# Kernel optimization log

Hardware: AMD Instinct MI355X
Metric: run time of the kernel (lower is better)

The kernel has to match this reference:

```python
import jax, jax.numpy as jnp
import numpy as np

H = 16          # num_heads
OUT = 256       # out_channels; projection width = 5*OUT
LN_EPS = 1e-5


def setup_inputs() -> dict:
    key = jax.random.key(0)
    ks = jax.random.split(key, 8)
    B, T, C = 2, 2048, 1024
    P = 5 * OUT
    sc = 1.0 / np.sqrt(C)
    x = jax.random.normal(ks[0], (B, T, C), dtype=jnp.float32)
    Wq = jax.random.normal(ks[1], (C, C), dtype=jnp.float32) * sc
    Wk = jax.random.normal(ks[2], (C, C), dtype=jnp.float32) * sc
    Wv = jax.random.normal(ks[3], (C, C), dtype=jnp.float32) * sc
    bq = jnp.zeros((C,), jnp.float32)
    bk = jnp.zeros((C,), jnp.float32)
    bv = jnp.zeros((C,), jnp.float32)
    gamma = jnp.zeros((1,), jnp.float32)  # nn.Parameter(torch.zeros(1))
    Wp = jax.random.normal(ks[4], (C, P), dtype=jnp.float32) * sc
    bp = jnp.zeros((P,), jnp.float32)
    ln_g = jnp.ones((P,), jnp.float32)
    ln_b = jnp.zeros((P,), jnp.float32)
    bez_p = jnp.array([0.0, 0.0, 1.0, 1.0], jnp.float32)  # cubic Bezier control points
    return dict(x=x, Wq=Wq, bq=bq, Wk=Wk, bk=bk, Wv=Wv, bv=bv, gamma=gamma,
                Wp=Wp, bp=bp, ln_g=ln_g, ln_b=ln_b, bez_p=bez_p)


def _bezier(z, p):
    # cubic Bezier evaluated at s = sigmoid(z), scalar control points p[0..3]
    s = jax.nn.sigmoid(z)
    u = 1.0 - s
    return (u * u * u) * p[0] + 3.0 * (u * u) * s * p[1] + 3.0 * u * (s * s) * p[2] + (s * s * s) * p[3]


def reference(x, Wq, bq, Wk, bk, Wv, bv, gamma, Wp, bp, ln_g, ln_b, bez_p):
    B, T, C = x.shape
    D = C // H
    # QKV projections -> [B, H, T, D]
    q = (x @ Wq + bq).reshape(B, T, H, D).transpose(0, 2, 1, 3)
    k = (x @ Wk + bk).reshape(B, T, H, D).transpose(0, 2, 1, 3)
    v = (x @ Wv + bv).reshape(B, T, H, D).transpose(0, 2, 1, 3)
    # scaled dot-product attention, full [B,H,T,T] scores (as in source)
    attn = jax.nn.softmax(jnp.einsum('bhtd,bhsd->bhts', q, k) / (D ** 0.5), axis=-1)
    out = jnp.einsum('bhts,bhsd->bhtd', attn, v).transpose(0, 2, 1, 3).reshape(B, T, C)
    out = gamma * out + x  # gated residual
    # projection: Linear -> LayerNorm -> BezierActivation
    h = out @ Wp + bp
    mu = jnp.mean(h, axis=-1, keepdims=True)
    var = jnp.mean(jnp.square(h - mu), axis=-1, keepdims=True)
    h = (h - mu) * jax.lax.rsqrt(var + LN_EPS) * ln_g + ln_b
    return _bezier(h, bez_p)
```

## Files before the change

### kernel.cpp

```cpp
#include <hip/hip_runtime.h>
#include <hip/hip_bf16.h>
#include <math.h>


#define H_ 16
#define D_ 64
#define B_ 2
#define T_ 2048
#define C_ 1024
#define P_ 1280
#define M_ 4096

#define PREP_CAST0 1280
#define PREP_QKV0  2304
#define PREP_GRID  5376

typedef __bf16 bf16_t;
typedef __bf16 v8bf __attribute__((ext_vector_type(8)));
typedef __bf16 v4bf __attribute__((ext_vector_type(4)));
typedef float  v4f  __attribute__((ext_vector_type(4)));

__device__ __forceinline__ void gload_lds16(const void* g, void* l) {
  __builtin_amdgcn_global_load_lds((const __attribute__((address_space(1))) void*)g,
                                   (__attribute__((address_space(3))) void*)l, 16, 0, 0);
}

__device__ __forceinline__ void stage64x64(const bf16_t* __restrict__ g, bf16_t* lds, int tid) {
#pragma unroll
  for (int i = 0; i < 2; ++i) {
    int off  = i * 4096 + tid * 16;
    int row  = off >> 7;
    int colb = off & 127;
    const char* gp = (const char*)g + (size_t)row * 2048 + colb;
    char* lp = (char*)lds + i * 4096 + (tid >> 6) * 1024;
    gload_lds16(gp, lp);
  }
}

template<int LD>
__device__ __forceinline__ void stage_tile128x32(const bf16_t* __restrict__ g, bf16_t* lds, int tid) {
#pragma unroll
  for (int i = 0; i < 2; ++i) {
    int off  = i * 4096 + tid * 16;
    int row  = off >> 6;
    int colb = off & 63;
    const char* gp = (const char*)(g + row * LD) + colb;
    char* lp = (char*)lds + i * 4096 + (tid >> 6) * 1024;
    gload_lds16(gp, lp);
  }
}

__device__ __forceinline__ void stage_f32_tile(const float* __restrict__ src, bf16_t* lds, int tid) {
  int row = tid >> 1, half = tid & 1;
  const float* xp = src + (size_t)row * C_ + half * 16;
  float4 f0 = *(const float4*)(xp);
  float4 f1 = *(const float4*)(xp + 4);
  float4 f2 = *(const float4*)(xp + 8);
  float4 f3 = *(const float4*)(xp + 12);
  v8bf lo = {(__bf16)f0.x, (__bf16)f0.y, (__bf16)f0.z, (__bf16)f0.w,
             (__bf16)f1.x, (__bf16)f1.y, (__bf16)f1.z, (__bf16)f1.w};
  v8bf hi = {(__bf16)f2.x, (__bf16)f2.y, (__bf16)f2.z, (__bf16)f2.w,
             (__bf16)f3.x, (__bf16)f3.y, (__bf16)f3.z, (__bf16)f3.w};
  *(v8bf*)(lds + row * 32 + half * 16)     = lo;
  *(v8bf*)(lds + row * 32 + half * 16 + 8) = hi;
}

__global__ __launch_bounds__(256) void prep_kernel(const float* __restrict__ Wp, bf16_t* __restrict__ WpT,
                                                   const float* __restrict__ x, bf16_t* __restrict__ pa,
                                                   const float* __restrict__ Wq, const float* __restrict__ Wk,
                                                   const float* __restrict__ Wv, bf16_t* __restrict__ WT,
                                                   const float* __restrict__ gamma) {
  __shared__ float tile[32][33];
  const int bid = blockIdx.x;
  const float* src;
  bf16_t* dst;
  int N, tile_id;
  if (bid < PREP_CAST0) {
    src = Wp; dst = WpT; N = P_; tile_id = bid;
  } else if (bid < PREP_QKV0) {
    int base = ((bid - PREP_CAST0) * 256 + threadIdx.x) * 16;
    float4 f0 = *(const float4*)(x + base);
    float4 f1 = *(const float4*)(x + base + 4);
    float4 f2 = *(const float4*)(x + base + 8);
    float4 f3 = *(const float4*)(x + base + 12);
    v8bf lo = {(__bf16)f0.x, (__bf16)f0.y, (__bf16)f0.z, (__bf16)f0.w,
               (__bf16)f1.x, (__bf16)f1.y, (__bf16)f1.z, (__bf16)f1.w};
    v8bf hi = {(__bf16)f2.x, (__bf16)f2.y, (__bf16)f2.z, (__bf16)f2.w,
               (__bf16)f3.x, (__bf16)f3.y, (__bf16)f3.z, (__bf16)f3.w};
    *(v8bf*)(pa + base)     = lo;
    *(v8bf*)(pa + base + 8) = hi;
    return;
  } else {
    if (gamma[0] == 0.0f) return;
    int b2 = bid - PREP_QKV0;
    int w = b2 >> 10;
    tile_id = b2 & 1023;
    src = (w == 0) ? Wq : (w == 1) ? Wk : Wv;
    dst = WT + (size_t)w * C_ * C_;
    N = C_;
  }
  const int nt = N / 32;
  const int n0 = (tile_id % nt) * 32, k0 = (tile_id / nt) * 32;
  const int tx = threadIdx.x & 31, ty = threadIdx.x >> 5;
#pragma unroll
  for (int i = 0; i < 32; i += 8)
    tile[ty + i][tx] = src[(size_t)(k0 + ty + i) * N + n0 + tx];
  __syncthreads();
#pragma unroll
  for (int i = 0; i < 32; i += 8)
    dst[(size_t)(n0 + ty + i) * C_ + k0 + tx] = (bf16_t)tile[tx][ty + i];
}

__global__ __launch_bounds__(256) void gemm_qkv(const float* __restrict__ x,
                                                const bf16_t* __restrict__ WT,
                                                const float* __restrict__ bq,
                                                const float* __restrict__ bk,
                                                const float* __restrict__ bv,
                                                bf16_t* __restrict__ q, bf16_t* __restrict__ k,
                                                bf16_t* __restrict__ v,
                                                const float* __restrict__ gamma) {
  if (gamma[0] == 0.0f) return;
  __shared__ alignas(16) bf16_t sA[128 * 32];
  __shared__ alignas(16) bf16_t sB[128 * 32];
  const int tid = threadIdx.x;
  const int m0  = blockIdx.y * 128;
  const int ng0 = blockIdx.x * 128;
  const int w   = ng0 >> 10;
  const int n0  = ng0 & 1023;
  const float*  Ax = x + (size_t)m0 * C_;
  const bf16_t* Bt = WT + (size_t)ng0 * C_;
  const int lane = tid & 63;
  const int wv   = tid >> 6;
  const int wr   = (wv >> 1) * 64;
  const int wc   = (wv & 1) * 64;
  const int kb   = (lane >> 4) * 8;
  const int fr   = lane & 15;
  v4f acc[4][4] = {};
  for (int k0 = 0; k0 < C_; k0 += 32) {
    stage_f32_tile(Ax + k0, sA, tid);
    stage_tile128x32<C_>(Bt + k0, sB, tid);
    __syncthreads();
    v8bf af[4], bfv[4];
#pragma unroll
    for (int f = 0; f < 4; ++f) {
      af[f]  = *(const v8bf*)(sA + (wr + f * 16 + fr) * 32 + kb);
      bfv[f] = *(const v8bf*)(sB + (wc + f * 16 + fr) * 32 + kb);
    }
#pragma unroll
    for (int i = 0; i < 4; ++i)
#pragma unroll
      for (int j = 0; j < 4; ++j)
        acc[i][j] = __builtin_amdgcn_mfma_f32_16x16x32_bf16(af[i], bfv[j], acc[i][j], 0, 0, 0);
    __syncthreads();
  }
  const float* bias = (w == 0) ? bq : (w == 1) ? bk : bv;
  bf16_t* outb = (w == 0) ? q : (w == 1) ? k : v;
#pragma unroll
  for (int fj = 0; fj < 4; ++fj) {
    int colL = n0 + wc + fj * 16 + fr;
    float bsv = bias[colL];
    int hh = colL >> 6, dd = colL & 63;
#pragma unroll
    for (int fi = 0; fi < 4; ++fi) {
#pragma unroll
      for (int i = 0; i < 4; ++i) {
        int m = m0 + wr + fi * 16 + (lane >> 4) * 4 + i;
        int bb = m >> 11, tt = m & 2047;
        outb[(((size_t)bb * H_ + hh) * T_ + tt) * D_ + dd] = (bf16_t)(acc[fi][fj][i] + bsv);
      }
    }
  }
}

__global__ __launch_bounds__(256) void attn_kernel(const bf16_t* __restrict__ q,
                                                   const bf16_t* __restrict__ k,
                                                   const bf16_t* __restrict__ v,
                                                   const float* __restrict__ x,
                                                   bf16_t* __restrict__ pa,
                                                   const float* __restrict__ gamma) {
  const float g = gamma[0];
  if (g == 0.0f) return;
  __shared__ alignas(16) bf16_t sP[4][16 * 32];
  const int tid = threadIdx.x, lane = tid & 63, wv = tid >> 6;
  const int bh = blockIdx.y;
  const int q0 = blockIdx.x * 64 + wv * 16;
  const bf16_t* Q = q + (size_t)bh * T_ * D_;
  const bf16_t* K = k + (size_t)bh * T_ * D_;
  const bf16_t* V = v + (size_t)bh * T_ * D_;
  const int fr = lane & 15, kb = (lane >> 4) * 8;
  v8bf qf[2];
  qf[0] = *(const v8bf*)(Q + (q0 + fr) * 64 + kb);
  qf[1] = *(const v8bf*)(Q + (q0 + fr) * 64 + 32 + kb);
  float mrow[4], lrow[4];
  v4f oacc[4] = {};
#pragma unroll
  for (int i = 0; i < 4; ++i) { mrow[i] = -1e30f; lrow[i] = 0.f; }
  for (int kv0 = 0; kv0 < T_; kv0 += 32) {
    v4f s[2] = {};
#pragma unroll
    for (int nf = 0; nf < 2; ++nf) {
      v8bf k0f = *(const v8bf*)(K + (kv0 + nf * 16 + fr) * 64 + kb);
      v8bf k1f = *(const v8bf*)(K + (kv0 + nf * 16 + fr) * 64 + 32 + kb);
      s[nf] = __builtin_amdgcn_mfma_f32_16x16x32_bf16(qf[0], k0f, s[nf], 0, 0, 0);
      s[nf] = __builtin_amdgcn_mfma_f32_16x16x32_bf16(qf[1], k1f, s[nf], 0, 0, 0);
    }
#pragma unroll
    for (int nf = 0; nf < 2; ++nf)
#pragma unroll
      for (int i = 0; i < 4; ++i) s[nf][i] *= 0.125f;
    float fac[4];
#pragma unroll
    for (int i = 0; i < 4; ++i) {
      float mx = fmaxf(s[0][i], s[1][i]);
      for (int off = 1; off < 16; off <<= 1) mx = fmaxf(mx, __shfl_xor(mx, off));
      float mn = fmaxf(mrow[i], mx);
      fac[i] = expf(mrow[i] - mn);
      mrow[i] = mn;
      float p0 = expf(s[0][i] - mn);
      float p1 = expf(s[1][i] - mn);
      s[0][i] = p0; s[1][i] = p1;
      float ts = p0 + p1;
      for (int off = 1; off < 16; off <<= 1) ts += __shfl_xor(ts, off);
      lrow[i] = lrow[i] * fac[i] + ts;
#pragma unroll
      for (int df = 0; df < 4; ++df) oacc[df][i] *= fac[i];
    }
    bf16_t* myP = &sP[wv][0];
#pragma unroll
    for (int nf = 0; nf < 2; ++nf)
#pragma unroll
      for (int i = 0; i < 4; ++i)
        myP[((lane >> 4) * 4 + i) * 32 + nf * 16 + fr] = (bf16_t)s[nf][i];
    __syncthreads();
    v8bf pf = *(const v8bf*)(myP + fr * 32 + kb);
#pragma unroll
    for (int df = 0; df < 4; ++df) {
      v8bf vf;
#pragma unroll
      for (int j = 0; j < 8; ++j) vf[j] = V[(size_t)(kv0 + kb + j) * 64 + df * 16 + fr];
      oacc[df] = __builtin_amdgcn_mfma_f32_16x16x32_bf16(pf, vf, oacc[df], 0, 0, 0);
    }
    __syncthreads();
  }
  const int b = bh >> 4, hh = bh & 15;
#pragma unroll
  for (int df = 0; df < 4; ++df)
#pragma unroll
    for (int i = 0; i < 4; ++i) {
      int qr = q0 + (lane >> 4) * 4 + i;
      size_t m = (size_t)b * T_ + qr;
      int c = hh * 64 + df * 16 + fr;
      float o = oacc[df][i] / lrow[i];
      float xv = x[m * C_ + c];
      pa[m * C_ + c] = (bf16_t)fmaf(g, o, xv);
    }
}

__global__ __launch_bounds__(256) void gemm_proj(const bf16_t* __restrict__ pa,
                                                 const bf16_t* __restrict__ WpT,
                                                 const float* __restrict__ bp,
                                                 bf16_t* __restrict__ h) {
  __shared__ alignas(16) bf16_t sA[64 * 64];
  __shared__ alignas(16) bf16_t sB[64 * 64];
  const int tid = threadIdx.x;
  const int bid = blockIdx.x;
  const int wg  = (bid & 7) * 160 + (bid >> 3);
  const int m0  = (wg / 20) * 64;
  const int n0  = (wg % 20) * 64;
  const bf16_t* A  = pa  + (size_t)m0 * C_;
  const bf16_t* Bt = WpT + (size_t)n0 * C_;
  const int lane = tid & 63;
  const int wv   = tid >> 6;
  const int wr   = (wv >> 1) * 32;
  const int wc   = (wv & 1) * 32;
  const int kb   = (lane >> 4) * 8;
  const int fr   = lane & 15;
  v4f acc[2][2] = {};
  for (int k0 = 0; k0 < C_; k0 += 64) {
    stage64x64(A + k0, sA, tid);
    stage64x64(Bt + k0, sB, tid);
    __syncthreads();
#pragma unroll
    for (int kc = 0; kc < 2; ++kc) {
      v8bf af[2], bfv[2];
#pragma unroll
      for (int f = 0; f < 2; ++f) {
        af[f]  = *(const v8bf*)(sA + (wr + f * 16 + fr) * 64 + kc * 32 + kb);
        bfv[f] = *(const v8bf*)(sB + (wc + f * 16 + fr) * 64 + kc * 32 + kb);
      }
#pragma unroll
      for (int i = 0; i < 2; ++i)
#pragma unroll
        for (int j = 0; j < 2; ++j)
          acc[i][j] = __builtin_amdgcn_mfma_f32_16x16x32_bf16(af[i], bfv[j], acc[i][j], 0, 0, 0);
    }
    __syncthreads();
  }
#pragma unroll
  for (int fj = 0; fj < 2; ++fj) {
    int n = n0 + wc + fj * 16 + fr;
    float bsv = bp[n];
#pragma unroll
    for (int fi = 0; fi < 2; ++fi) {
#pragma unroll
      for (int i = 0; i < 4; ++i) {
        int m = m0 + wr + fi * 16 + (lane >> 4) * 4 + i;
        h[(size_t)m * P_ + n] = (bf16_t)(acc[fi][fj][i] + bsv);
      }
    }
  }
}

__global__ __launch_bounds__(256) void ln_bezier(const bf16_t* __restrict__ h,
                                                 const float* __restrict__ ln_g,
                                                 const float* __restrict__ ln_b,
                                                 const float* __restrict__ bez,
                                                 float* __restrict__ out) {
  const int lane = threadIdx.x & 63;
  const int row  = blockIdx.x * 4 + (threadIdx.x >> 6);
  const bf16_t* hr = h + (size_t)row * P_;
  float v[20];
  float s = 0.f, ss = 0.f;
#pragma unroll
  for (int p = 0; p < 5; ++p) {
    v4bf hv = *(const v4bf*)(hr + p * 256 + lane * 4);
#pragma unroll
    for (int j = 0; j < 4; ++j) {
      float f = (float)hv[j];
      v[p * 4 + j] = f;
      s += f; ss += f * f;
    }
  }
#pragma unroll
  for (int off = 1; off < 64; off <<= 1) {
    s  += __shfl_xor(s, off);
    ss += __shfl_xor(ss, off);
  }
  const float inv = 1.0f / (float)P_;
  float mu = s * inv;
  float var = ss * inv - mu * mu;
  float rstd = rsqrtf(var + 1e-5f);
  float p0 = bez[0], p1 = bez[1], p2 = bez[2], p3 = bez[3];
#pragma unroll
  for (int p = 0; p < 5; ++p) {
    int c = p * 256 + lane * 4;
    float4 g4 = *(const float4*)(ln_g + c);
    float4 b4 = *(const float4*)(ln_b + c);
    float4 o4;
    float gg[4] = {g4.x, g4.y, g4.z, g4.w};
    float bb[4] = {b4.x, b4.y, b4.z, b4.w};
    float oo[4];
#pragma unroll
    for (int j = 0; j < 4; ++j) {
      float y = (v[p * 4 + j] - mu) * rstd * gg[j] + bb[j];
      float sg = 1.0f / (1.0f + expf(-y));
      float u = 1.0f - sg;
      oo[j] = u * u * u * p0 + 3.0f * u * u * sg * p1 + 3.0f * u * sg * sg * p2 + sg * sg * sg * p3;
    }
    o4.x = oo[0]; o4.y = oo[1]; o4.z = oo[2]; o4.w = oo[3];
    *(float4*)(out + (size_t)row * P_ + c) = o4;
  }
}

extern "C" void kernel_launch(void* const* d_in, const int* in_sizes, int n_in,
                              void* d_out, int out_size, void* d_ws, size_t ws_size,
                              hipStream_t stream) {
  const float* x     = (const float*)d_in[0];
  const float* Wq    = (const float*)d_in[1];
  const float* bq    = (const float*)d_in[2];
  const float* Wk    = (const float*)d_in[3];
  const float* bk    = (const float*)d_in[4];
  const float* Wv    = (const float*)d_in[5];
  const float* bv    = (const float*)d_in[6];
  const float* gamma = (const float*)d_in[7];
  const float* Wp    = (const float*)d_in[8];
  const float* bp    = (const float*)d_in[9];
  const float* ln_g  = (const float*)d_in[10];
  const float* ln_b  = (const float*)d_in[11];
  const float* bez   = (const float*)d_in[12];
  float* out = (float*)d_out;

  char* ws = (char*)d_ws;
  bf16_t* qb  = (bf16_t*)(ws);
  bf16_t* kb_ = (bf16_t*)(ws + (size_t)8  * 1048576);
  bf16_t* vb  = (bf16_t*)(ws + (size_t)16 * 1048576);
  bf16_t* WT  = (bf16_t*)(ws + (size_t)24 * 1048576);
  bf16_t* pa  = (bf16_t*)(ws + (size_t)30 * 1048576);
  bf16_t* WpT = (bf16_t*)(ws + (size_t)38 * 1048576);
  bf16_t* hb  = (bf16_t*)(ws + (size_t)41 * 1048576);

  prep_kernel<<<PREP_GRID, 256, 0, stream>>>(Wp, WpT, x, pa, Wq, Wk, Wv, WT, gamma);
  gemm_qkv<<<dim3(24, 32), 256, 0, stream>>>(x, WT, bq, bk, bv, qb, kb_, vb, gamma);
  attn_kernel<<<dim3(32, 32), 256, 0, stream>>>(qb, kb_, vb, x, pa, gamma);
  gemm_proj<<<1280, 256, 0, stream>>>(pa, WpT, bp, hb);
  ln_bezier<<<1024, 256, 0, stream>>>(hb, ln_g, ln_b, bez, out);
}
```

Before: 49.33 us.

## Retile projection GEMM to 128x160 blocks with double-buffered swizzled LDS

Replaces the 64x64-tile projection GEMM with 128x160 tiles, 512 threads (8 waves each computing 32x80), and double-buffered LDS staging so the global-to-LDS copy of the next K slice overlaps MFMA work on the current one. An XOR swizzle on LDS column chunks is meant to reduce bank conflicts on fragment reads. Fewer, larger blocks (256 instead of 1280) increase operand reuse but leave fewer blocks than a full-chip multiple and raise register and LDS pressure per block.

```diff
diff --git a/kernel.cpp b/kernel.cpp
--- a/kernel.cpp
+++ b/kernel.cpp
@@ -15,6 +15,10 @@
 #define PREP_QKV0  2304
 #define PREP_GRID  5376
 
+#define BM 128
+#define BN 160
+#define BKp 64
+
 typedef __bf16 bf16_t;
 typedef __bf16 v8bf __attribute__((ext_vector_type(8)));
 typedef __bf16 v4bf __attribute__((ext_vector_type(4)));
@@ -23,18 +27,6 @@
 __device__ __forceinline__ void gload_lds16(const void* g, void* l) {
   __builtin_amdgcn_global_load_lds((const __attribute__((address_space(1))) void*)g,
                                    (__attribute__((address_space(3))) void*)l, 16, 0, 0);
-}
-
-__device__ __forceinline__ void stage64x64(const bf16_t* __restrict__ g, bf16_t* lds, int tid) {
-#pragma unroll
-  for (int i = 0; i < 2; ++i) {
-    int off  = i * 4096 + tid * 16;
-    int row  = off >> 7;
-    int colb = off & 127;
-    const char* gp = (const char*)g + (size_t)row * 2048 + colb;
-    char* lp = (char*)lds + i * 4096 + (tid >> 6) * 1024;
-    gload_lds16(gp, lp);
-  }
 }
 
 template<int LD>
@@ -256,55 +248,93 @@
     }
 }
 
-__global__ __launch_bounds__(256) void gemm_proj(const bf16_t* __restrict__ pa,
+__global__ __launch_bounds__(512) void gemm_proj(const bf16_t* __restrict__ pa,
                                                  const bf16_t* __restrict__ WpT,
                                                  const float* __restrict__ bp,
                                                  bf16_t* __restrict__ h) {
-  __shared__ alignas(16) bf16_t sA[64 * 64];
-  __shared__ alignas(16) bf16_t sB[64 * 64];
-  const int tid = threadIdx.x;
+  __shared__ alignas(16) bf16_t sA[2][BM * BKp];
+  __shared__ alignas(16) bf16_t sB[2][BN * BKp];
+  const int tid = threadIdx.x, lane = tid & 63, wv = tid >> 6;
   const int bid = blockIdx.x;
-  const int wg  = (bid & 7) * 160 + (bid >> 3);
-  const int m0  = (wg / 20) * 64;
-  const int n0  = (wg % 20) * 64;
-  const bf16_t* A  = pa  + (size_t)m0 * C_;
-  const bf16_t* Bt = WpT + (size_t)n0 * C_;
-  const int lane = tid & 63;
-  const int wv   = tid >> 6;
-  const int wr   = (wv >> 1) * 32;
-  const int wc   = (wv & 1) * 32;
-  const int kb   = (lane >> 4) * 8;
-  const int fr   = lane & 15;
-  v4f acc[2][2] = {};
-  for (int k0 = 0; k0 < C_; k0 += 64) {
-    stage64x64(A + k0, sA, tid);
-    stage64x64(Bt + k0, sB, tid);
+  const int wg  = (bid & 7) * 32 + (bid >> 3);
+  const int m0  = (wg >> 3) * BM;
+  const int n0  = (wg & 7) * BN;
+  const int wr = (wv >> 1) * 32;
+  const int wc = (wv & 1) * 80;
+  const int fr = lane & 15, q = lane >> 4;
+  const int srow = lane >> 3;
+  const int scolb = (((lane & 7) ^ srow) << 4);
+  const bf16_t* Abase = pa  + (size_t)m0 * C_;
+  const bf16_t* Bbase = WpT + (size_t)n0 * C_;
+
+  v4f acc[2][5] = {};
+
+#define STAGE_PROJ(buf, kk)                                                          \
+  do {                                                                               \
+    for (int c = wv; c < 36; c += 8) {                                               \
+      if (c < 16) {                                                                  \
+        int row = c * 8 + srow;                                                      \
+        const char* gp = (const char*)(Abase + (size_t)row * C_ + (kk)) + scolb;     \
+        gload_lds16(gp, (char*)&sA[buf][0] + c * 1024);                              \
+      } else {                                                                       \
+        int row = (c - 16) * 8 + srow;                                               \
+        const char* gp = (const char*)(Bbase + (size_t)row * C_ + (kk)) + scolb;     \
+        gload_lds16(gp, (char*)&sB[buf][0] + (c - 16) * 1024);                       \
+      }                                                                              \
+    }                                                                                \
+  } while (0)
+
+#define COMPUTE_PROJ(buf)                                                            \
+  do {                                                                               \
+    _Pragma("unroll")                                                                \
+    for (int kc = 0; kc < 2; ++kc) {                                                 \
+      const int c16 = kc * 4 + q;                                                    \
+      const int sw  = (c16 ^ (fr & 7)) * 8;                                          \
+      v8bf av[2], bv5[5];                                                            \
+      _Pragma("unroll")                                                              \
+      for (int fi = 0; fi < 2; ++fi)                                                 \
+        av[fi] = *(const v8bf*)(&sA[buf][0] + (wr + fi * 16 + fr) * BKp + sw);       \
+      _Pragma("unroll")                                                              \
+      for (int fj = 0; fj < 5; ++fj)                                                 \
+        bv5[fj] = *(const v8bf*)(&sB[buf][0] + (wc + fj * 16 + fr) * BKp + sw);      \
+      _Pragma("unroll")                                                              \
+      for (int fi = 0; fi < 2; ++fi)                                                 \
+        _Pragma("unroll")                                                            \
+        for (int fj = 0; fj < 5; ++fj)                                               \
+          acc[fi][fj] = __builtin_amdgcn_mfma_f32_16x16x32_bf16(av[fi], bv5[fj],     \
+                                                                acc[fi][fj], 0, 0, 0);\
+    }                                                                                \
+  } while (0)
+
+  STAGE_PROJ(0, 0);
+  __syncthreads();
+  int cur = 0;
+#pragma unroll 1
+  for (int t = 0; t < 15; ++t) {
+    if (cur == 0) {
+      STAGE_PROJ(1, (t + 1) * BKp);
+      COMPUTE_PROJ(0);
+    } else {
+      STAGE_PROJ(0, (t + 1) * BKp);
+      COMPUTE_PROJ(1);
+    }
     __syncthreads();
-#pragma unroll
-    for (int kc = 0; kc < 2; ++kc) {
-      v8bf af[2], bfv[2];
-#pragma unroll
-      for (int f = 0; f < 2; ++f) {
-        af[f]  = *(const v8bf*)(sA + (wr + f * 16 + fr) * 64 + kc * 32 + kb);
-        bfv[f] = *(const v8bf*)(sB + (wc + f * 16 + fr) * 64 + kc * 32 + kb);
-      }
-#pragma unroll
-      for (int i = 0; i < 2; ++i)
-#pragma unroll
-        for (int j = 0; j < 2; ++j)
-          acc[i][j] = __builtin_amdgcn_mfma_f32_16x16x32_bf16(af[i], bfv[j], acc[i][j], 0, 0, 0);
-    }
-    __syncthreads();
-  }
-#pragma unroll
-  for (int fj = 0; fj < 2; ++fj) {
+    cur ^= 1;
+  }
+  if (cur == 0) COMPUTE_PROJ(0); else COMPUTE_PROJ(1);
+
+#undef STAGE_PROJ
+#undef COMPUTE_PROJ
+
+#pragma unroll
+  for (int fj = 0; fj < 5; ++fj) {
     int n = n0 + wc + fj * 16 + fr;
     float bsv = bp[n];
 #pragma unroll
     for (int fi = 0; fi < 2; ++fi) {
 #pragma unroll
       for (int i = 0; i < 4; ++i) {
-        int m = m0 + wr + fi * 16 + (lane >> 4) * 4 + i;
+        int m = m0 + wr + fi * 16 + q * 4 + i;
         h[(size_t)m * P_ + n] = (bf16_t)(acc[fi][fj][i] + bsv);
       }
     }
@@ -392,6 +422,6 @@
   prep_kernel<<<PREP_GRID, 256, 0, stream>>>(Wp, WpT, x, pa, Wq, Wk, Wv, WT, gamma);
   gemm_qkv<<<dim3(24, 32), 256, 0, stream>>>(x, WT, bq, bk, bv, qb, kb_, vb, gamma);
   attn_kernel<<<dim3(32, 32), 256, 0, stream>>>(qb, kb_, vb, x, pa, gamma);
-  gemm_proj<<<1280, 256, 0, stream>>>(pa, WpT, bp, hb);
+  gemm_proj<<<256, 512, 0, stream>>>(pa, WpT, bp, hb);
   ln_bezier<<<1024, 256, 0, stream>>>(hb, ln_g, ln_b, bez, out);
 }
```

New measurement: 44.14 us. -10.5%, faster.
